# Kernel tuning notes

Hardware: AMD Instinct MI355X
Metric: run time of the kernel (lower is better)

## Reference

```python
import jax, jax.numpy as jnp
import numpy as np

RC = 6.0            # cosine cutoff radius (Angstrom)
N_ANGULAR = 128     # module init arg; output dim = 3*N_ANGULAR
EPS = 1e-12


def cosine_cutoff(d):
    # Behler-style cosine cutoff: 0.5*(cos(pi*d/rc)+1) for d < rc, else 0
    return jnp.where(d < RC, 0.5 * (jnp.cos(jnp.pi * d / RC) + 1.0), 0.0)


def setup_inputs() -> dict:
    key = jax.random.key(0)
    k1, k2, k3, k4 = jax.random.split(key, 4)
    B, N, M = 8, 4096, 96
    L = 20.0  # box length
    positions = jax.random.uniform(k1, (B, N, 3), dtype=jnp.float32) * L
    cell = jnp.tile(jnp.eye(3, dtype=jnp.float32) * L, (B, 1, 1))
    neighbors = jax.random.randint(k2, (B, N, M), 0, N, dtype=jnp.int32)
    offsets = jax.random.randint(k3, (B, N, M, 3), -1, 2).astype(jnp.float32)
    mask = (jax.random.uniform(k4, (B, N, M)) > 0.1).astype(jnp.float32)
    return {"positions": positions, "cell": cell, "offsets": offsets,
            "mask": mask, "neighbors": neighbors}


def reference(positions, cell, offsets, mask, neighbors):
    B, N, M = neighbors.shape
    # gather neighbor positions: pos_j[b,n,m,:] = positions[b, neighbors[b,n,m], :]
    idx = neighbors.reshape(B, N * M)
    pos_j = jnp.take_along_axis(positions, idx[:, :, None], axis=1).reshape(B, N, M, 3)
    # displacement vectors with periodic offsets (offsets in cell coordinates)
    dis_vec = pos_j - positions[:, :, None, :] + jnp.einsum('bnmi,bij->bnmj', offsets, cell)
    distances = jnp.sqrt(jnp.sum(dis_vec * dis_vec, axis=-1) + EPS)  # [B,N,M]
    # cutoff / distance, zeroed where mask == 0
    cut = jnp.where(mask != 0.0, cosine_cutoff(distances) / distances, 0.0)
    # sort neighbors by descending cut value, gather cut-weighted vectors in that order
    order = jnp.argsort(-cut, axis=-1)                       # [B,N,M]
    cut_vec = cut[..., None] * dis_vec                       # [B,N,M,3]
    cut_vec = jnp.take_along_axis(cut_vec, order[..., None], axis=2)
    cut_vec = cut_vec.reshape(B, N, M * 3)
    # scatter into zero-padded descriptor of width 3*n_angular
    f = jnp.zeros((B, N, N_ANGULAR * 3), dtype=positions.dtype)
    f = f.at[:, :, : M * 3].set(cut_vec)
    return f
```

## Files before the change

kernel.cpp:

```cpp
#include <hip/hip_runtime.h>
#include <math.h>

#define M_NB  96
#define OUT_W 384
#define PPBLK 8

__global__ __launch_bounds__(256) void deepmd_angular_kernel(
    const float* __restrict__ positions,
    const float* __restrict__ cell,
    const float* __restrict__ offsets,
    const float* __restrict__ mask,
    const int*   __restrict__ neighbors,
    float*       __restrict__ out,
    int N)
{
    __shared__ float cut_s[4][2][M_NB];

    const int tid  = threadIdx.x;
    const int wv   = tid >> 6;
    const int lane = tid & 63;
    const int h    = lane >> 5;
    const int t    = lane & 31;

    const int pblk = blockIdx.x * PPBLK;
    const int b    = pblk / N;
    const int p    = pblk + wv * 2 + h;

    float4* orow = (float4*)(out + (size_t)(pblk + wv * 2) * OUT_W);
    const float4 z4 = make_float4(0.f, 0.f, 0.f, 0.f);
    orow[lane]       = z4;
    orow[lane + 64]  = z4;
    orow[lane + 128] = z4;

    const float* cb = cell + (size_t)b * 9;
    const float c00 = cb[0], c01 = cb[1], c02 = cb[2];
    const float c10 = cb[3], c11 = cb[4], c12 = cb[5];
    const float c20 = cb[6], c21 = cb[7], c22 = cb[8];

    const float pix = positions[(size_t)p * 3 + 0];
    const float piy = positions[(size_t)p * 3 + 1];
    const float piz = positions[(size_t)p * 3 + 2];

    int jn[3]; float mk[3], o0[3], o1[3], o2[3];
    #pragma unroll
    for (int i = 0; i < 3; ++i) {
        const long e = (long)p * M_NB + t + 32 * i;
        jn[i] = neighbors[e];
        mk[i] = mask[e];
        o0[i] = offsets[e * 3 + 0];
        o1[i] = offsets[e * 3 + 1];
        o2[i] = offsets[e * 3 + 2];
    }

    const long posb = (long)b * N * 3;
    float dx[3], dy[3], dz[3], cut[3];
    #pragma unroll
    for (int i = 0; i < 3; ++i) {
        const float* pj = positions + posb + (long)jn[i] * 3;
        dx[i] = pj[0] - pix + o0[i] * c00 + o1[i] * c10 + o2[i] * c20;
        dy[i] = pj[1] - piy + o0[i] * c01 + o1[i] * c11 + o2[i] * c21;
        dz[i] = pj[2] - piz + o0[i] * c02 + o1[i] * c12 + o2[i] * c22;
        const float d = sqrtf(dx[i] * dx[i] + dy[i] * dy[i] + dz[i] * dz[i] + 1e-12f);
        float c = 0.f;
        if (mk[i] != 0.f && d < 6.f)
            c = 0.5f * (cosf(d * 0.52359877559829887f) + 1.f) / d;
        cut[i] = c;
        cut_s[wv][h][t + 32 * i] = c;
    }

    if (cut[0] != 0.f || cut[1] != 0.f || cut[2] != 0.f) {
        __threadfence_block();
        #pragma unroll
        for (int i = 0; i < 3; ++i) {
            if (cut[i] == 0.f) continue;
            const int m = t + 32 * i;
            int rank = 0;
            const float4* c4 = (const float4*)cut_s[wv][h];
            #pragma unroll
            for (int k4 = 0; k4 < M_NB / 4; ++k4) {
                const float4 c = c4[k4];
                const int k = 4 * k4;
                rank += (c.x > cut[i]) || (c.x == cut[i] && k + 0 < m);
                rank += (c.y > cut[i]) || (c.y == cut[i] && k + 1 < m);
                rank += (c.z > cut[i]) || (c.z == cut[i] && k + 2 < m);
                rank += (c.w > cut[i]) || (c.w == cut[i] && k + 3 < m);
            }
            float* dst = out + (size_t)p * OUT_W + rank * 3;
            dst[0] = cut[i] * dx[i];
            dst[1] = cut[i] * dy[i];
            dst[2] = cut[i] * dz[i];
        }
    }
}

extern "C" void kernel_launch(void* const* d_in, const int* in_sizes, int n_in,
                              void* d_out, int out_size, void* d_ws, size_t ws_size,
                              hipStream_t stream) {
    const float* positions = (const float*)d_in[0];
    const float* cell      = (const float*)d_in[1];
    const float* offsets   = (const float*)d_in[2];
    const float* mask      = (const float*)d_in[3];
    const int*   neighbors = (const int*)d_in[4];
    float*       out       = (float*)d_out;

    const int BN = in_sizes[0] / 3;
    const int B  = in_sizes[1] / 9;
    const int N  = BN / B;

    dim3 block(256, 1, 1);
    dim3 grid(BN / PPBLK, 1, 1);
    deepmd_angular_kernel<<<grid, block, 0, stream>>>(
        positions, cell, offsets, mask, neighbors, out, N);
}
```

Baseline: 136.7 us.

## Software-pipeline per-wave atom loop and stage output rows in shared memory

```diff
diff --git a/kernel.cpp b/kernel.cpp
--- a/kernel.cpp
+++ b/kernel.cpp
@@ -3,9 +3,38 @@
 
 #define M_NB  96
 #define OUT_W 384
-#define PPBLK 8
+#define WPB   4
+#define NITER 4
 
-__global__ __launch_bounds__(256) void deepmd_angular_kernel(
+struct Items {
+    int   jA, jB;
+    float mkA, mkB;
+    float oA0, oA1, oA2, oB0, oB1, oB2;
+};
+
+__device__ __forceinline__ void load_items(Items& it_,
+    const int* __restrict__ nb, const float* __restrict__ mk,
+    const float* __restrict__ of, long q, int mA, int mB)
+{
+    const long eA = q * M_NB + mA, eB = q * M_NB + mB;
+    it_.jA  = nb[eA];       it_.jB  = nb[eB];
+    it_.mkA = mk[eA];       it_.mkB = mk[eB];
+    it_.oA0 = of[eA * 3];   it_.oA1 = of[eA * 3 + 1]; it_.oA2 = of[eA * 3 + 2];
+    it_.oB0 = of[eB * 3];   it_.oB1 = of[eB * 3 + 1]; it_.oB2 = of[eB * 3 + 2];
+}
+
+struct Gath { float ax, ay, az, bx, by, bz; };
+
+__device__ __forceinline__ void load_gath(Gath& g,
+    const float* __restrict__ pos, long posb, int jA, int jB)
+{
+    const float* pa = pos + posb + (long)jA * 3;
+    const float* pb = pos + posb + (long)jB * 3;
+    g.ax = pa[0]; g.ay = pa[1]; g.az = pa[2];
+    g.bx = pb[0]; g.by = pb[1]; g.bz = pb[2];
+}
+
+__global__ __launch_bounds__(64 * WPB, 8) void deepmd_angular_kernel(
     const float* __restrict__ positions,
     const float* __restrict__ cell,
     const float* __restrict__ offsets,
@@ -14,82 +43,108 @@
     float*       __restrict__ out,
     int N)
 {
-    __shared__ float cut_s[4][2][M_NB];
+    __shared__ float cut_s[WPB][M_NB];
+    __shared__ float out_s[WPB][OUT_W];
 
     const int tid  = threadIdx.x;
     const int wv   = tid >> 6;
     const int lane = tid & 63;
-    const int h    = lane >> 5;
-    const int t    = lane & 31;
+    const int l32  = lane & 31;
+    const bool low = lane < 32;
+    const int mA   = lane;
+    const int mB   = 64 + l32;
 
-    const int pblk = blockIdx.x * PPBLK;
-    const int b    = pblk / N;
-    const int p    = pblk + wv * 2 + h;
-
-    float4* orow = (float4*)(out + (size_t)(pblk + wv * 2) * OUT_W);
-    const float4 z4 = make_float4(0.f, 0.f, 0.f, 0.f);
-    orow[lane]       = z4;
-    orow[lane + 64]  = z4;
-    orow[lane + 128] = z4;
+    const int qbase = blockIdx.x * (WPB * NITER) + wv;
+    const int b     = __builtin_amdgcn_readfirstlane(qbase) / N;
 
     const float* cb = cell + (size_t)b * 9;
     const float c00 = cb[0], c01 = cb[1], c02 = cb[2];
     const float c10 = cb[3], c11 = cb[4], c12 = cb[5];
     const float c20 = cb[6], c21 = cb[7], c22 = cb[8];
+    const long posb = (long)b * N * 3;
 
-    const float pix = positions[(size_t)p * 3 + 0];
-    const float piy = positions[(size_t)p * 3 + 1];
-    const float piz = positions[(size_t)p * 3 + 2];
+    Items cur, nxt;
+    Gath  gc, gn;
+    load_items(cur, neighbors, mask, offsets, qbase, mA, mB);
+    load_gath(gc, positions, posb, cur.jA, cur.jB);
+    load_items(nxt, neighbors, mask, offsets, qbase + WPB, mA, mB);
 
-    int jn[3]; float mk[3], o0[3], o1[3], o2[3];
+    const float4 z4 = make_float4(0.f, 0.f, 0.f, 0.f);
+
     #pragma unroll
-    for (int i = 0; i < 3; ++i) {
-        const long e = (long)p * M_NB + t + 32 * i;
-        jn[i] = neighbors[e];
-        mk[i] = mask[e];
-        o0[i] = offsets[e * 3 + 0];
-        o1[i] = offsets[e * 3 + 1];
-        o2[i] = offsets[e * 3 + 2];
-    }
+    for (int it = 0; it < NITER; ++it) {
+        const long q  = qbase + (long)WPB * it;
+        const int  uq = __builtin_amdgcn_readfirstlane((int)q);
 
-    const long posb = (long)b * N * 3;
-    float dx[3], dy[3], dz[3], cut[3];
-    #pragma unroll
-    for (int i = 0; i < 3; ++i) {
-        const float* pj = positions + posb + (long)jn[i] * 3;
-        dx[i] = pj[0] - pix + o0[i] * c00 + o1[i] * c10 + o2[i] * c20;
-        dy[i] = pj[1] - piy + o0[i] * c01 + o1[i] * c11 + o2[i] * c21;
-        dz[i] = pj[2] - piz + o0[i] * c02 + o1[i] * c12 + o2[i] * c22;
-        const float d = sqrtf(dx[i] * dx[i] + dy[i] * dy[i] + dz[i] * dz[i] + 1e-12f);
-        float c = 0.f;
-        if (mk[i] != 0.f && d < 6.f)
-            c = 0.5f * (cosf(d * 0.52359877559829887f) + 1.f) / d;
-        cut[i] = c;
-        cut_s[wv][h][t + 32 * i] = c;
-    }
+        Items nxt2;
+        if (it + 2 < NITER)
+            load_items(nxt2, neighbors, mask, offsets, qbase + (long)WPB * (it + 2), mA, mB);
+        if (it + 1 < NITER)
+            load_gath(gn, positions, posb, nxt.jA, nxt.jB);
 
-    if (cut[0] != 0.f || cut[1] != 0.f || cut[2] != 0.f) {
-        __threadfence_block();
-        #pragma unroll
-        for (int i = 0; i < 3; ++i) {
-            if (cut[i] == 0.f) continue;
-            const int m = t + 32 * i;
+        const float* pu = positions + (size_t)uq * 3;
+        const float pix = pu[0], piy = pu[1], piz = pu[2];
+
+        const float dxA = gc.ax - pix + cur.oA0 * c00 + cur.oA1 * c10 + cur.oA2 * c20;
+        const float dyA = gc.ay - piy + cur.oA0 * c01 + cur.oA1 * c11 + cur.oA2 * c21;
+        const float dzA = gc.az - piz + cur.oA0 * c02 + cur.oA1 * c12 + cur.oA2 * c22;
+        const float dxB = gc.bx - pix + cur.oB0 * c00 + cur.oB1 * c10 + cur.oB2 * c20;
+        const float dyB = gc.by - piy + cur.oB0 * c01 + cur.oB1 * c11 + cur.oB2 * c21;
+        const float dzB = gc.bz - piz + cur.oB0 * c02 + cur.oB1 * c12 + cur.oB2 * c22;
+
+        const float dA = sqrtf(dxA * dxA + dyA * dyA + dzA * dzA + 1e-12f);
+        const float dB = sqrtf(dxB * dxB + dyB * dyB + dzB * dzB + 1e-12f);
+
+        float cutA = 0.f, cutB = 0.f;
+        if (cur.mkA != 0.f && dA < 6.f)
+            cutA = 0.5f * (cosf(dA * 0.52359877559829887f) + 1.f) / dA;
+        if (cur.mkB != 0.f && dB < 6.f)
+            cutB = 0.5f * (cosf(dB * 0.52359877559829887f) + 1.f) / dB;
+
+        float4* os4 = (float4*)out_s[wv];
+        os4[lane] = z4;
+        if (low) os4[64 + l32] = z4;
+        cut_s[wv][mA] = cutA;
+        if (low) cut_s[wv][mB] = cutB;
+
+        if (cutA != 0.f) {
             int rank = 0;
-            const float4* c4 = (const float4*)cut_s[wv][h];
+            const float4* c4 = (const float4*)cut_s[wv];
             #pragma unroll
             for (int k4 = 0; k4 < M_NB / 4; ++k4) {
                 const float4 c = c4[k4];
                 const int k = 4 * k4;
-                rank += (c.x > cut[i]) || (c.x == cut[i] && k + 0 < m);
-                rank += (c.y > cut[i]) || (c.y == cut[i] && k + 1 < m);
-                rank += (c.z > cut[i]) || (c.z == cut[i] && k + 2 < m);
-                rank += (c.w > cut[i]) || (c.w == cut[i] && k + 3 < m);
+                rank += (c.x > cutA) || (c.x == cutA && k + 0 < mA);
+                rank += (c.y > cutA) || (c.y == cutA && k + 1 < mA);
+                rank += (c.z > cutA) || (c.z == cutA && k + 2 < mA);
+                rank += (c.w > cutA) || (c.w == cutA && k + 3 < mA);
             }
-            float* dst = out + (size_t)p * OUT_W + rank * 3;
-            dst[0] = cut[i] * dx[i];
-            dst[1] = cut[i] * dy[i];
-            dst[2] = cut[i] * dz[i];
+            out_s[wv][rank * 3 + 0] = cutA * dxA;
+            out_s[wv][rank * 3 + 1] = cutA * dyA;
+            out_s[wv][rank * 3 + 2] = cutA * dzA;
         }
+        if (low && cutB != 0.f) {
+            int rank = 0;
+            const float4* c4 = (const float4*)cut_s[wv];
+            #pragma unroll
+            for (int k4 = 0; k4 < M_NB / 4; ++k4) {
+                const float4 c = c4[k4];
+                const int k = 4 * k4;
+                rank += (c.x > cutB) || (c.x == cutB && k + 0 < mB);
+                rank += (c.y > cutB) || (c.y == cutB && k + 1 < mB);
+                rank += (c.z > cutB) || (c.z == cutB && k + 2 < mB);
+                rank += (c.w > cutB) || (c.w == cutB && k + 3 < mB);
+            }
+            out_s[wv][rank * 3 + 0] = cutB * dxB;
+            out_s[wv][rank * 3 + 1] = cutB * dyB;
+            out_s[wv][rank * 3 + 2] = cutB * dzB;
+        }
+
+        float4* orow = (float4*)(out + (size_t)q * OUT_W);
+        orow[lane] = os4[lane];
+        if (low) orow[64 + l32] = os4[64 + l32];
+
+        cur = nxt; gc = gn; nxt = nxt2;
     }
 }
 
@@ -107,8 +162,8 @@
     const int B  = in_sizes[1] / 9;
     const int N  = BN / B;
 
-    dim3 block(256, 1, 1);
-    dim3 grid(BN / PPBLK, 1, 1);
+    dim3 block(64 * WPB, 1, 1);
+    dim3 grid(BN / (WPB * NITER), 1, 1);
     deepmd_angular_kernel<<<grid, block, 0, stream>>>(
         positions, cell, offsets, mask, neighbors, out, N);
 }
```

Result: slower. 144.7 us (+5.8%).
